# Performance work log

Measured on AMD Instinct MI355X. Metric: run time of the kernel, lower is better.

## Reference

```python
import jax, jax.numpy as jnp
import numpy as np
from jax import lax

E, H, V, S, T, B = 128, 254, 32000, 50, 50, 64


def setup_inputs() -> dict:
    key = jax.random.key(0)
    ks = jax.random.split(key, 14)
    sc = 0.05
    n = lambda k, shape: jax.random.normal(k, shape, dtype=jnp.float32) * sc
    return {
        "src": jax.random.randint(ks[0], (S, B), 0, V),
        "trg": jax.random.randint(ks[1], (T, B), 0, V),
        "emb_enc": n(ks[2], (V, E)),
        "W_ih_e": n(ks[3], (3 * H, E)),
        "W_hh_e": n(ks[4], (3 * H, H)),
        "b_ih_e": n(ks[5], (3 * H,)),
        "b_hh_e": n(ks[6], (3 * H,)),
        "emb_dec": n(ks[7], (V, E)),
        "W_ih_d": n(ks[8], (3 * H, E + H)),
        "W_hh_d": n(ks[9], (3 * H, H)),
        "b_ih_d": n(ks[10], (3 * H,)),
        "b_hh_d": n(ks[11], (3 * H,)),
        "W_out": n(ks[12], (V, E + 2 * H)),
        "b_out": n(ks[13], (V,)),
    }


def _gru_cell(x, h, W_ih, W_hh, b_ih, b_hh):
    # PyTorch GRU cell: gates ordered [r, z, n]
    gi = x @ W_ih.T + b_ih            # [B, 3H]
    gh = h @ W_hh.T + b_hh            # [B, 3H]
    i_r, i_z, i_n = jnp.split(gi, 3, axis=-1)
    h_r, h_z, h_n = jnp.split(gh, 3, axis=-1)
    r = jax.nn.sigmoid(i_r + h_r)
    z = jax.nn.sigmoid(i_z + h_z)
    n = jnp.tanh(i_n + r * h_n)
    return (1.0 - z) * n + z * h


def reference(src, trg, emb_enc, W_ih_e, W_hh_e, b_ih_e, b_hh_e,
              emb_dec, W_ih_d, W_hh_d, b_ih_d, b_hh_d, W_out, b_out):
    dt = emb_enc.dtype
    # --- Encoder: GRU over src (dropout = identity in eval) ---
    enc_emb = emb_enc[src]                       # [S, B, E]
    h0 = jnp.zeros((B, H), dtype=dt)

    def enc_step(h, x):
        h2 = _gru_cell(x, h, W_ih_e, W_hh_e, b_ih_e, b_hh_e)
        return h2, None

    context, _ = lax.scan(enc_step, h0, enc_emb)  # [B, H]

    # --- Decoder: teacher forcing (ratio=1.0) => scan over trg[:-1] ---
    dec_emb = emb_dec[trg[:-1]]                  # [T-1, B, E]

    def dec_step(h, e):
        xc = jnp.concatenate([e, context], axis=-1)          # [B, E+H]
        h2 = _gru_cell(xc, h, W_ih_d, W_hh_d, b_ih_d, b_hh_d)
        feat = jnp.concatenate([h2, context, e], axis=-1)    # [B, E+2H]
        pred = feat @ W_out.T + b_out                        # [B, V]
        return h2, pred

    _, preds = lax.scan(dec_step, context, dec_emb)  # [T-1, B, V]
    outputs = jnp.concatenate(
        [jnp.zeros((1, B, V), dtype=preds.dtype), preds], axis=0)  # [T, B, V]
    return outputs
```

## Files before the change

### kernel.cpp

```cpp
#include <hip/hip_runtime.h>
#include <cstdint>
#include <cstddef>

typedef unsigned short u16;
typedef unsigned int u32;
typedef __attribute__((ext_vector_type(8))) short bf16x8;
typedef __attribute__((ext_vector_type(4))) float f32x4;

#define AS1 __attribute__((address_space(1)))
#define AS3 __attribute__((address_space(3)))

__device__ __forceinline__ float bf2f(u16 u){ u32 x = ((u32)u)<<16; float f; __builtin_memcpy(&f,&x,4); return f; }
__device__ __forceinline__ u16 f2bf(float f){ u32 x; __builtin_memcpy(&x,&f,4); u32 r=(x+0x7FFFu+((x>>16)&1u))>>16; return (u16)r; }

__device__ __forceinline__ float fast_sig(float x){
  return __fdividef(1.f, 1.f + __expf(-x));
}
__device__ __forceinline__ float fast_tanh(float x){
  float e = __expf(2.f*x);
  return 1.f - __fdividef(2.f, e + 1.f);
}

__device__ __forceinline__ void dev_store_u16(u16* p, u16 v){
  __hip_atomic_store(p, v, __ATOMIC_RELAXED, __HIP_MEMORY_SCOPE_AGENT);
}
__device__ __forceinline__ void dev_store_u32(u32* p, u32 v){
  __hip_atomic_store(p, v, __ATOMIC_RELAXED, __HIP_MEMORY_SCOPE_AGENT);
}


__global__ void zero_bytes(uint4* p, size_t n16){
  size_t i = (size_t)blockIdx.x*blockDim.x + threadIdx.x;
  size_t st = (size_t)gridDim.x*blockDim.x;
  uint4 z; z.x=0u; z.y=0u; z.z=0u; z.w=0u;
  for (; i<n16; i+=st) p[i]=z;
}

__global__ void pad_convert_g(const float* __restrict__ src, int src_ld, int c0, int vcols,
                              u16* __restrict__ dst, int dcols){
  int i = blockIdx.x*256 + threadIdx.x;
  int tot = 768*dcols;
  if (i >= tot) return;
  int p = i/dcols, c = i - p*dcols;
  int wv = p/96, rem = p - wv*96, sec = rem>>5, u = rem&31;
  int j = wv*32 + u;
  float v = 0.f;
  if (j < 254 && c < vcols) v = src[(size_t)(sec*254 + j)*src_ld + c0 + c];
  dst[i] = f2bf(v);
}

__global__ void pad_bias_comb(const float* __restrict__ ih, const float* __restrict__ hh,
                              float* __restrict__ dst){
  int p = blockIdx.x*256 + threadIdx.x;
  if (p >= 768) return;
  int wv = p/96, rem = p - wv*96, sec = rem>>5, u = rem&31;
  int j = wv*32 + u;
  float v = 0.f;
  if (j < 254){ v = ih[sec*254 + j]; if (sec < 2) v += hh[sec*254 + j]; }
  dst[p] = v;
}

__global__ void pad_bias_g(const float* __restrict__ src, float* __restrict__ dst){
  int p = blockIdx.x*256 + threadIdx.x;
  if (p >= 768) return;
  int wv = p/96, rem = p - wv*96, sec = rem>>5, u = rem&31;
  int j = wv*32 + u;
  dst[p] = (j<254) ? src[sec*254 + j] : 0.f;
}

__global__ void gather_enc(const int* __restrict__ idx, const float* __restrict__ emb, u16* __restrict__ dst){
  int i = blockIdx.x*256 + threadIdx.x;
  int r = i>>7, k = i&127;
  dst[i] = f2bf(emb[(size_t)idx[r]*128 + k]);
}

__global__ void gather_dec(const int* __restrict__ idx, const float* __restrict__ emb,
                           u16* __restrict__ dst, u16* __restrict__ feat){
  int i = blockIdx.x*256 + threadIdx.x;
  int r = i>>7, k = i&127;
  u16 v = 0;
  if (r < 3136) v = f2bf(emb[(size_t)idx[r]*128 + k]);
  dst[i] = v;
  if (r < 3136) feat[(size_t)r*640 + 508 + k] = v;
}


__global__ __launch_bounds__(256) void gemm_bt16(
  const u16* __restrict__ A, int lda,
  const u16* __restrict__ B, int ldb,
  u16* __restrict__ C, long long ldc,
  const float* __restrict__ bias,
  int K, int Mtiles, int Mstore)
{
  __shared__ __align__(16) u16 Abuf[2][128*64];
  __shared__ __align__(16) u16 Bbuf[2][128*64];
  const int t = threadIdx.x;
  const int w = t>>6, l = t&63;
  const int wm = w>>1, wn = w&1;
  const int mt = blockIdx.x % Mtiles, nt = blockIdx.x / Mtiles;
  const int m0 = mt<<7, n0 = nt<<7;

  const int lr = l>>3, lg = l&7;

  auto stage = [&](const u16* __restrict__ G, int ld, int base0, int k0, u16* Lbuf){
    #pragma unroll
    for (int i=0;i<4;++i){
      const int rbase = i*32 + w*8;
      const int r = rbase + lr;
      const int gsw = lg ^ (r&7);
      __builtin_amdgcn_global_load_lds(
        (const AS1 void*)(G + (size_t)(base0+r)*ld + k0 + gsw*8),
        (AS3 void*)(Lbuf + rbase*64), 16, 0, 0);
    }
  };

  f32x4 acc[4][4] = {};
  const int ksteps = K>>6;

  stage(A, lda, m0, 0, Abuf[0]);
  stage(B, ldb, n0, 0, Bbuf[0]);
  asm volatile("s_waitcnt vmcnt(0)" ::: "memory");
  __syncthreads();

  for (int ks=0; ks<ksteps; ++ks){
    const int cb = ks&1;
    if (ks+1 < ksteps){
      stage(A, lda, m0, (ks+1)<<6, Abuf[cb^1]);
      stage(B, ldb, n0, (ks+1)<<6, Bbuf[cb^1]);
    }
    const u16* Al = Abuf[cb];
    const u16* Bl = Bbuf[cb];
    #pragma unroll
    for (int kk=0;kk<2;++kk){
      const int ko = kk*32 + (l>>4)*8;
      bf16x8 af[4], bfr[4];
      #pragma unroll
      for (int m=0;m<4;++m){
        const int row = wm*64+m*16+(l&15);
        af[m] = *(const bf16x8*)&Al[row*64 + (ko ^ ((row&7)<<3))];
      }
      #pragma unroll
      for (int n=0;n<4;++n){
        const int row = wn*64+n*16+(l&15);
        bfr[n] = *(const bf16x8*)&Bl[row*64 + (ko ^ ((row&7)<<3))];
      }
      #pragma unroll
      for (int m=0;m<4;++m)
        #pragma unroll
        for (int n=0;n<4;++n)
          acc[m][n] = __builtin_amdgcn_mfma_f32_16x16x32_bf16(af[m], bfr[n], acc[m][n], 0,0,0);
    }
    asm volatile("s_waitcnt vmcnt(0)" ::: "memory");
    __syncthreads();
  }

  float bv[4];
  #pragma unroll
  for (int n=0;n<4;++n) bv[n] = bias[n0 + wn*64 + n*16 + (l&15)];
  #pragma unroll
  for (int m=0;m<4;++m){
    const int rb = m0 + wm*64 + m*16 + (l>>4)*4;
    #pragma unroll
    for (int n=0;n<4;++n){
      const int col = n0 + wn*64 + n*16 + (l&15);
      #pragma unroll
      for (int r=0;r<4;++r){
        const int rr = rb + r;
        if (rr < Mstore) C[(size_t)rr*ldc + col] = f2bf(acc[m][n][r] + bv[n]);
      }
    }
  }
}


__global__ __launch_bounds__(512,1) void fused_scan_gemm(
  const u16* Whhe, const u16* Whhd, const u16* Wihdc,
  const float* bhhe, const float* bhhd,
  const u16* enc_gi, const u16* dec_gi,
  u16* feat, u16* wout_b, const float* W_out,
  float* Cg, const float* b_out, u32* ctr)
{
  __shared__ __align__(16) char smem[115200];
  const int t = threadIdx.x;
  const int w = t>>6, l = t&63;

  if (blockIdx.x < 4){
    const int g = blockIdx.x;
    const int la = l&15, q = l>>4;
    const int brow0 = g*16;

    u16* hb   = (u16*)smem;
    u16* gib  = (u16*)(smem + 16896);
    u16* ctxb = (u16*)(smem + 90624);

    bf16x8 Bf[48];

    auto loadW = [&](const u16* __restrict__ W){
      #pragma unroll
      for (int nt=0; nt<6; ++nt)
        #pragma unroll
        for (int kk=0; kk<8; ++kk)
          Bf[nt*8+kk] = *(const bf16x8*)&W[(size_t)(w*96 + nt*16 + la)*256 + kk*32 + q*8];
    };

    auto stage = [&](const u16* __restrict__ gsrc, int step, u16* dstL){
      const u16* src = gsrc + (size_t)(step*64 + brow0)*768;
      #pragma unroll
      for (int i=0;i<3;++i){
        const int off = i*4096 + w*512;
        __builtin_amdgcn_global_load_lds((const AS1 void*)(src + off + l*8),
                                         (AS3 void*)(dstL + off), 16, 0, 0);
      }
    };

    auto mm = [&](const u16* hsrc, f32x4* acc){
      #pragma unroll
      for (int kk=0; kk<8; ++kk){
        bf16x8 a = *(const bf16x8*)&hsrc[la*264 + kk*32 + q*8];
        #pragma unroll
        for (int nt=0; nt<6; ++nt)
          acc[nt] = __builtin_amdgcn_mfma_f32_16x16x32_bf16(a, Bf[nt*8+kk], acc[nt], 0,0,0);
      }
    };

    for (int i=t; i<2*16*264; i+=512) hb[i] = 0;
    loadW(Whhe);
    float bn[2];
    #pragma unroll
    for (int tl=0; tl<2; ++tl) bn[tl] = bhhe[w*96 + tl*16 + la + 64];
    stage(enc_gi, 0, gib);
    stage(enc_gi, 1, gib + 12288);
    asm volatile("s_waitcnt vmcnt(0) lgkmcnt(0)" ::: "memory");
    __builtin_amdgcn_s_barrier();

    #pragma unroll 1
    for (int s=0; s<50; ++s){
      const int hc = s&1;
      const u16* gcur = gib + (s%3)*12288;
      if (s+2 < 50) stage(enc_gi, s+2, gib + ((s+2)%3)*12288);
      f32x4 acc[6] = {};
      mm(hb + hc*4224, acc);
      #pragma unroll
      for (int tl=0; tl<2; ++tl){
        const int pb = w*96 + tl*16 + la;
        const int j  = w*32 + tl*16 + la;
        #pragma unroll
        for (int r=0;r<4;++r){
          const int b = q*4 + r;
          const float gir = bf2f(gcur[b*768 + pb]);
          const float giz = bf2f(gcur[b*768 + pb + 32]);
          const float gin = bf2f(gcur[b*768 + pb + 64]);
          const float ho = bf2f(hb[hc*4224 + b*264 + j]);
          const float rg = fast_sig(gir + acc[tl][r]);
          const float zg = fast_sig(giz + acc[2+tl][r]);
          const float ng = fast_tanh(gin + rg*(acc[4+tl][r] + bn[tl]));
          hb[(hc^1)*4224 + b*264 + j] = f2bf((1.f-zg)*ng + zg*ho);
        }
      }
      if (s+2 < 50) asm volatile("s_waitcnt vmcnt(3) lgkmcnt(0)" ::: "memory");
      else          asm volatile("s_waitcnt vmcnt(0) lgkmcnt(0)" ::: "memory");
      __builtin_amdgcn_s_barrier();
    }

    stage(dec_gi, 0, gib);
    stage(dec_gi, 1, gib + 12288);

    loadW(Wihdc);
    {
      f32x4 acc[6] = {};
      mm(hb, acc);
      #pragma unroll
      for (int nt=0; nt<6; ++nt)
        #pragma unroll
        for (int r=0;r<4;++r)
          ctxb[(q*4+r)*768 + w*96 + nt*16 + la] = f2bf(acc[nt][r]);
    }

    #pragma unroll 1
    for (int i=t; i<49*2048; i+=512){
      const int tt = i>>11, rem = i&2047, b = rem>>7, c2 = rem&127;
      if (c2 < 127){
        u32 v = *(const u32*)&hb[b*264 + c2*2];
        dev_store_u32((u32*)&feat[(size_t)(tt*64 + brow0 + b)*640 + 254 + c2*2], v);
      }
    }

    loadW(Whhd);
    #pragma unroll
    for (int tl=0; tl<2; ++tl) bn[tl] = bhhd[w*96 + tl*16 + la + 64];
    asm volatile("s_waitcnt vmcnt(0) lgkmcnt(0)" ::: "memory");
    __builtin_amdgcn_s_barrier();

    #pragma unroll 1
    for (int tt=0; tt<49; ++tt){
      const int hc = tt&1;
      const u16* gcur = gib + (tt%3)*12288;
      if (tt+2 < 49) stage(dec_gi, tt+2, gib + ((tt+2)%3)*12288);
      f32x4 acc[6] = {};
      mm(hb + hc*4224, acc);
      #pragma unroll
      for (int tl=0; tl<2; ++tl){
        const int pb = w*96 + tl*16 + la;
        const int j  = w*32 + tl*16 + la;
        #pragma unroll
        for (int r=0;r<4;++r){
          const int b = q*4 + r;
          const float gir = bf2f(gcur[b*768 + pb])      + bf2f(ctxb[b*768 + pb]);
          const float giz = bf2f(gcur[b*768 + pb + 32]) + bf2f(ctxb[b*768 + pb + 32]);
          const float gin = bf2f(gcur[b*768 + pb + 64]) + bf2f(ctxb[b*768 + pb + 64]);
          const float ho = bf2f(hb[hc*4224 + b*264 + j]);
          const float rg = fast_sig(gir + acc[tl][r]);
          const float zg = fast_sig(giz + acc[2+tl][r]);
          const float ng = fast_tanh(gin + rg*(acc[4+tl][r] + bn[tl]));
          const float h2 = (1.f-zg)*ng + zg*ho;
          const u16 hbv = f2bf(h2);
          hb[(hc^1)*4224 + b*264 + j] = hbv;
          if (j < 254) dev_store_u16(&feat[(size_t)(tt*64 + brow0 + b)*640 + j], hbv);
        }
      }
      if (tt+2 < 49) asm volatile("s_waitcnt vmcnt(11) lgkmcnt(0)" ::: "memory");
      else           asm volatile("s_waitcnt vmcnt(8) lgkmcnt(0)"  ::: "memory");
      __builtin_amdgcn_s_barrier();
      if (t==0) dev_store_u32(&ctr[g], (u32)tt);
    }
    asm volatile("s_waitcnt vmcnt(0)" ::: "memory");
    __syncthreads();
    if (t==0) dev_store_u32(&ctr[g], 49u);
    return;
  }

  const int bg = blockIdx.x - 4;
  const int wm = w>>2, wn = w&3;
  const int la = l&15, q = l>>4;
  const int lr = l>>3, lg = l&7;

  u16* AL = (u16*)smem;
  u16* BL = (u16*)(smem + 32768);

  if (bg < 125){
    const int n0c = bg<<8;
    #pragma unroll 1
    for (int i=t; i<256*80; i+=512){
      const int r = i/80, c8 = (i - r*80)<<3;
      u16 o[8];
      #pragma unroll
      for (int jj=0;jj<8;++jj){
        const int c = c8 + jj;
        o[jj] = (c < 636) ? f2bf(W_out[(size_t)(n0c+r)*636 + c]) : (u16)0;
      }
      u32* dst = (u32*)&wout_b[(size_t)(n0c+r)*640 + c8];
      const u32* sv = (const u32*)o;
      #pragma unroll
      for (int jj=0;jj<4;++jj) dev_store_u32(&dst[jj], sv[jj]);
    }
    asm volatile("s_waitcnt vmcnt(0)" ::: "memory");
    __syncthreads();
    if (t==0) dev_store_u32(&ctr[32 + bg], 1u);
  }

  const int nsleep = 1 + (bg&3);
  #pragma unroll 1
  for (int tau = bg; tau < 3125; tau += 248){
    const int mt = tau/125, nt = tau - mt*125;
    const int m0 = mt<<7, n0 = nt<<8;
    const u32 need = (u32)((2*mt+2 < 49) ? (2*mt+2) : 49);

    if (w==0){
      int cnt = 0;
      while (true){
        u32 v  = (l<4) ? __hip_atomic_load(&ctr[l], __ATOMIC_RELAXED, __HIP_MEMORY_SCOPE_AGENT) : 0xFFFFFFFFu;
        u32 wf = (l==4) ? __hip_atomic_load(&ctr[32 + nt], __ATOMIC_RELAXED, __HIP_MEMORY_SCOPE_AGENT) : 1u;
        if (__all((int)((v >= need) && (wf != 0u)))) break;
        for (int z=0; z<nsleep; ++z) __builtin_amdgcn_s_sleep(16);
        if (++cnt > (1<<22)) break;
      }
    }
    __syncthreads();

    auto stageA = [&](int k0, int buf){
      #pragma unroll
      for (int i=0;i<2;++i){
        const int rbase = i*64 + w*8;
        const int r = rbase + lr;
        __builtin_amdgcn_global_load_lds(
          (const AS1 void*)(feat + (size_t)(m0+r)*640 + k0 + ((lg^lr)<<3)),
          (AS3 void*)(AL + buf*8192 + rbase*64), 16, 0, 0);
      }
    };
    auto stageB = [&](int k0, int buf){
      #pragma unroll
      for (int i=0;i<4;++i){
        const int rbase = i*64 + w*8;
        const int r = rbase + lr;
        __builtin_amdgcn_global_load_lds(
          (const AS1 void*)(wout_b + (size_t)(n0+r)*640 + k0 + ((lg^lr)<<3)),
          (AS3 void*)(BL + buf*16384 + rbase*64), 16, 0, 0);
      }
    };

    f32x4 acc[4][4] = {};
    stageA(0,0); stageB(0,0);
    asm volatile("s_waitcnt vmcnt(0)" ::: "memory");
    __syncthreads();

    #pragma unroll 1
    for (int ks=0; ks<10; ++ks){
      const int cb = ks&1;
      if (ks < 9){ stageA((ks+1)<<6, cb^1); stageB((ks+1)<<6, cb^1); }
      const u16* Alp = AL + cb*8192;
      const u16* Blp = BL + cb*16384;
      #pragma unroll
      for (int kk=0;kk<2;++kk){
        const int ko = kk*32 + q*8;
        bf16x8 af[4], bfr[4];
        #pragma unroll
        for (int m=0;m<4;++m){
          const int row = wm*64 + m*16 + la;
          af[m] = *(const bf16x8*)&Alp[row*64 + (ko ^ ((row&7)<<3))];
        }
        #pragma unroll
        for (int n=0;n<4;++n){
          const int row = wn*64 + n*16 + la;
          bfr[n] = *(const bf16x8*)&Blp[row*64 + (ko ^ ((row&7)<<3))];
        }
        #pragma unroll
        for (int m=0;m<4;++m)
          #pragma unroll
          for (int n=0;n<4;++n)
            acc[m][n] = __builtin_amdgcn_mfma_f32_16x16x32_bf16(af[m], bfr[n], acc[m][n], 0,0,0);
      }
      asm volatile("s_waitcnt vmcnt(0)" ::: "memory");
      __syncthreads();
    }

    float bv[4];
    #pragma unroll
    for (int n=0;n<4;++n) bv[n] = b_out[n0 + wn*64 + n*16 + la];
    #pragma unroll
    for (int m=0;m<4;++m){
      const int rb = m0 + wm*64 + m*16 + q*4;
      #pragma unroll
      for (int n=0;n<4;++n){
        const int col = n0 + wn*64 + n*16 + la;
        #pragma unroll
        for (int r=0;r<4;++r){
          const int rr = rb + r;
          if (rr < 3136)
            __builtin_nontemporal_store(acc[m][n][r] + bv[n], &Cg[(size_t)rr*32000 + col]);
        }
      }
    }
  }
}


extern "C" void kernel_launch(void* const* d_in, const int* in_sizes, int n_in,
                              void* d_out, int out_size, void* d_ws, size_t ws_size,
                              hipStream_t stream) {
  const int*   src     = (const int*)d_in[0];
  const int*   trg     = (const int*)d_in[1];
  const float* emb_enc = (const float*)d_in[2];
  const float* W_ih_e  = (const float*)d_in[3];
  const float* W_hh_e  = (const float*)d_in[4];
  const float* b_ih_e  = (const float*)d_in[5];
  const float* b_hh_e  = (const float*)d_in[6];
  const float* emb_dec = (const float*)d_in[7];
  const float* W_ih_d  = (const float*)d_in[8];
  const float* W_hh_d  = (const float*)d_in[9];
  const float* b_ih_d  = (const float*)d_in[10];
  const float* b_hh_d  = (const float*)d_in[11];
  const float* W_out   = (const float*)d_in[12];
  const float* b_out   = (const float*)d_in[13];
  float* out = (float*)d_out;

  char* basep = (char*)d_ws;
  size_t off = 0;
  auto take = [&](size_t b)->char*{ char* p = basep + off; off = (off + b + 255) & ~(size_t)255; return p; };
  u16* feat    = (u16*)take(4096000);
  u32* ctr     = (u32*)take(4096);
  u16* wout_b  = (u16*)take(40960000);
  u16* wihe_b  = (u16*)take(196608);
  u16* wihde_b = (u16*)take(196608);
  u16* wihdc_b = (u16*)take(393216);
  u16* whhe_b  = (u16*)take(393216);
  u16* whhd_b  = (u16*)take(393216);
  u16* encx_b  = (u16*)take(819200);
  u16* dece_b  = (u16*)take(819200);
  u16* enc_gi  = (u16*)take(4915200);
  u16* dec_gi  = (u16*)take(4915200);
  float* bihe_p = (float*)take(3072);
  float* bihd_p = (float*)take(3072);
  float* bhhe_p = (float*)take(3072);
  float* bhhd_p = (float*)take(3072);
  (void)in_sizes; (void)n_in; (void)out_size; (void)ws_size;

  zero_bytes<<<1, 256, 0, stream>>>((uint4*)ctr, (size_t)(4096/16));
  zero_bytes<<<2000, 256, 0, stream>>>((uint4*)out, (size_t)(8192000/16));

  pad_convert_g<<<384, 256, 0, stream>>>(W_ih_e, 128,   0, 128, wihe_b, 128);
  pad_convert_g<<<384, 256, 0, stream>>>(W_ih_d, 382,   0, 128, wihde_b, 128);
  pad_convert_g<<<768, 256, 0, stream>>>(W_ih_d, 382, 128, 254, wihdc_b, 256);
  pad_convert_g<<<768, 256, 0, stream>>>(W_hh_e, 254,   0, 254, whhe_b, 256);
  pad_convert_g<<<768, 256, 0, stream>>>(W_hh_d, 254,   0, 254, whhd_b, 256);

  pad_bias_comb<<<3, 256, 0, stream>>>(b_ih_e, b_hh_e, bihe_p);
  pad_bias_comb<<<3, 256, 0, stream>>>(b_ih_d, b_hh_d, bihd_p);
  pad_bias_g<<<3, 256, 0, stream>>>(b_hh_e, bhhe_p);
  pad_bias_g<<<3, 256, 0, stream>>>(b_hh_d, bhhd_p);

  gather_enc<<<1600, 256, 0, stream>>>(src, emb_enc, encx_b);
  gather_dec<<<1600, 256, 0, stream>>>(trg, emb_dec, dece_b, feat);

  gemm_bt16<<<25*6, 256, 0, stream>>>(encx_b, 128, wihe_b, 128, enc_gi, (long long)768, bihe_p, 128, 25, 3200);
  gemm_bt16<<<25*6, 256, 0, stream>>>(dece_b, 128, wihde_b, 128, dec_gi, (long long)768, bihd_p, 128, 25, 3200);

  fused_scan_gemm<<<252, 512, 0, stream>>>(whhe_b, whhd_b, wihdc_b, bhhe_p, bhhd_p,
                                           enc_gi, dec_gi, feat, wout_b, W_out,
                                           out + (size_t)64*32000, b_out, ctr);
}
```

Measured before the change: 518.3 us.

## Transpose input-gate precompute layout and batch feature stores out of GRU recurrence

The input-projection GEMMs now produce gate pre-activations transposed (gate-major, [768 x 3200]) with bias applied per row, so the recurrent blocks can stage them and read four batch values per lane as one vector load. The decoder context projection is folded into dec_gi once before the recurrence, which removes the per-step context reads and frees LDS. The hidden state is carried in registers instead of being re-read from LDS. Per-element feature stores are replaced by one wide 64-bit copy of the previous step's hidden row, issued early in the next step. The cost is an extra pass over dec_gi in global memory before the decoder loop, and the waitcnt bookkeeping becomes tighter.

```diff
diff --git a/kernel.cpp b/kernel.cpp
--- a/kernel.cpp
+++ b/kernel.cpp
@@ -4,8 +4,10 @@
 
 typedef unsigned short u16;
 typedef unsigned int u32;
+typedef unsigned long long u64;
 typedef __attribute__((ext_vector_type(8))) short bf16x8;
 typedef __attribute__((ext_vector_type(4))) float f32x4;
+typedef __attribute__((ext_vector_type(4))) unsigned short u16x4;
 
 #define AS1 __attribute__((address_space(1)))
 #define AS3 __attribute__((address_space(3)))
@@ -25,6 +27,9 @@
   __hip_atomic_store(p, v, __ATOMIC_RELAXED, __HIP_MEMORY_SCOPE_AGENT);
 }
 __device__ __forceinline__ void dev_store_u32(u32* p, u32 v){
+  __hip_atomic_store(p, v, __ATOMIC_RELAXED, __HIP_MEMORY_SCOPE_AGENT);
+}
+__device__ __forceinline__ void dev_store_u64(u64* p, u64 v){
   __hip_atomic_store(p, v, __ATOMIC_RELAXED, __HIP_MEMORY_SCOPE_AGENT);
 }
 
@@ -154,19 +159,19 @@
     __syncthreads();
   }
 
-  float bv[4];
-  #pragma unroll
-  for (int n=0;n<4;++n) bv[n] = bias[n0 + wn*64 + n*16 + (l&15)];
   #pragma unroll
   for (int m=0;m<4;++m){
     const int rb = m0 + wm*64 + m*16 + (l>>4)*4;
     #pragma unroll
-    for (int n=0;n<4;++n){
-      const int col = n0 + wn*64 + n*16 + (l&15);
-      #pragma unroll
-      for (int r=0;r<4;++r){
-        const int rr = rb + r;
-        if (rr < Mstore) C[(size_t)rr*ldc + col] = f2bf(acc[m][n][r] + bv[n]);
+    for (int r=0;r<4;++r){
+      const int rr = rb + r;
+      if (rr < Mstore){
+        const float bvr = bias[rr];
+        #pragma unroll
+        for (int n=0;n<4;++n){
+          const int col = n0 + wn*64 + n*16 + (l&15);
+          C[(size_t)rr*ldc + col] = f2bf(acc[m][n][r] + bvr);
+        }
       }
     }
   }
@@ -176,11 +181,11 @@
 __global__ __launch_bounds__(512,1) void fused_scan_gemm(
   const u16* Whhe, const u16* Whhd, const u16* Wihdc,
   const float* bhhe, const float* bhhd,
-  const u16* enc_gi, const u16* dec_gi,
+  const u16* enc_gi, u16* dec_gi,
   u16* feat, u16* wout_b, const float* W_out,
   float* Cg, const float* b_out, u32* ctr)
 {
-  __shared__ __align__(16) char smem[115200];
+  __shared__ __align__(16) char smem[98304];
   const int t = threadIdx.x;
   const int w = t>>6, l = t&63;
 
@@ -189,9 +194,8 @@
     const int la = l&15, q = l>>4;
     const int brow0 = g*16;
 
-    u16* hb   = (u16*)smem;
-    u16* gib  = (u16*)(smem + 16896);
-    u16* ctxb = (u16*)(smem + 90624);
+    u16* hb  = (u16*)smem;
+    u16* gib = (u16*)(smem + 16896);
 
     bf16x8 Bf[48];
 
@@ -204,12 +208,14 @@
     };
 
     auto stage = [&](const u16* __restrict__ gsrc, int step, u16* dstL){
-      const u16* src = gsrc + (size_t)(step*64 + brow0)*768;
+      const int colbase = step*64 + brow0 + ((l&1)<<3);
       #pragma unroll
       for (int i=0;i<3;++i){
-        const int off = i*4096 + w*512;
-        __builtin_amdgcn_global_load_lds((const AS1 void*)(src + off + l*8),
-                                         (AS3 void*)(dstL + off), 16, 0, 0);
+        const int rbase = (w*3 + i)*32;
+        const int row = rbase + (l>>1);
+        __builtin_amdgcn_global_load_lds(
+          (const AS1 void*)(gsrc + (size_t)row*3200 + colbase),
+          (AS3 void*)(dstL + rbase*16), 16, 0, 0);
       }
     };
 
@@ -228,6 +234,7 @@
     float bn[2];
     #pragma unroll
     for (int tl=0; tl<2; ++tl) bn[tl] = bhhe[w*96 + tl*16 + la + 64];
+    float hreg[8] = {};
     stage(enc_gi, 0, gib);
     stage(enc_gi, 1, gib + 12288);
     asm volatile("s_waitcnt vmcnt(0) lgkmcnt(0)" ::: "memory");
@@ -236,25 +243,26 @@
     #pragma unroll 1
     for (int s=0; s<50; ++s){
       const int hc = s&1;
-      const u16* gcur = gib + (s%3)*12288;
+      const u16* gT = gib + (s%3)*12288;
       if (s+2 < 50) stage(enc_gi, s+2, gib + ((s+2)%3)*12288);
       f32x4 acc[6] = {};
       mm(hb + hc*4224, acc);
       #pragma unroll
       for (int tl=0; tl<2; ++tl){
-        const int pb = w*96 + tl*16 + la;
+        const int pr = w*96 + tl*16 + la;
         const int j  = w*32 + tl*16 + la;
+        u16x4 g_r = *(const u16x4*)&gT[pr*16 + q*4];
+        u16x4 g_z = *(const u16x4*)&gT[(pr+32)*16 + q*4];
+        u16x4 g_n = *(const u16x4*)&gT[(pr+64)*16 + q*4];
         #pragma unroll
         for (int r=0;r<4;++r){
           const int b = q*4 + r;
-          const float gir = bf2f(gcur[b*768 + pb]);
-          const float giz = bf2f(gcur[b*768 + pb + 32]);
-          const float gin = bf2f(gcur[b*768 + pb + 64]);
-          const float ho = bf2f(hb[hc*4224 + b*264 + j]);
-          const float rg = fast_sig(gir + acc[tl][r]);
-          const float zg = fast_sig(giz + acc[2+tl][r]);
-          const float ng = fast_tanh(gin + rg*(acc[4+tl][r] + bn[tl]));
-          hb[(hc^1)*4224 + b*264 + j] = f2bf((1.f-zg)*ng + zg*ho);
+          const float rg = fast_sig(bf2f(g_r[r]) + acc[tl][r]);
+          const float zg = fast_sig(bf2f(g_z[r]) + acc[2+tl][r]);
+          const float ng = fast_tanh(bf2f(g_n[r]) + rg*(acc[4+tl][r] + bn[tl]));
+          const float h2 = (1.f-zg)*ng + zg*hreg[tl*4+r];
+          hreg[tl*4+r] = h2;
+          hb[(hc^1)*4224 + b*264 + j] = f2bf(h2);
         }
       }
       if (s+2 < 50) asm volatile("s_waitcnt vmcnt(3) lgkmcnt(0)" ::: "memory");
@@ -262,10 +270,8 @@
       __builtin_amdgcn_s_barrier();
     }
 
-    stage(dec_gi, 0, gib);
-    stage(dec_gi, 1, gib + 12288);
-
     loadW(Wihdc);
+    u16* ctxT = gib + 2*12288;
     {
       f32x4 acc[6] = {};
       mm(hb, acc);
@@ -273,8 +279,31 @@
       for (int nt=0; nt<6; ++nt)
         #pragma unroll
         for (int r=0;r<4;++r)
-          ctxb[(q*4+r)*768 + w*96 + nt*16 + la] = f2bf(acc[nt][r]);
-    }
+          ctxT[(w*96 + nt*16 + la)*16 + q*4 + r] = f2bf(acc[nt][r]);
+    }
+    asm volatile("s_waitcnt lgkmcnt(0)" ::: "memory");
+    __builtin_amdgcn_s_barrier();
+
+    #pragma unroll 1
+    for (int idx=t; idx<768*49; idx+=512){
+      const int p = idx/49, tt2 = idx - p*49;
+      u16* gp = dec_gi + (size_t)p*3200 + tt2*64 + brow0;
+      uint4 a0 = *(uint4*)gp, a1 = *((uint4*)gp + 1);
+      uint4 c0 = *(uint4*)&ctxT[p*16], c1 = *((uint4*)&ctxT[p*16] + 1);
+      auto addbf = [](u32 x, u32 y)->u32{
+        u32 lo = (u32)f2bf(bf2f((u16)(x&0xffff)) + bf2f((u16)(y&0xffff)));
+        u32 hi = (u32)f2bf(bf2f((u16)(x>>16))    + bf2f((u16)(y>>16)));
+        return lo | (hi<<16);
+      };
+      a0.x=addbf(a0.x,c0.x); a0.y=addbf(a0.y,c0.y); a0.z=addbf(a0.z,c0.z); a0.w=addbf(a0.w,c0.w);
+      a1.x=addbf(a1.x,c1.x); a1.y=addbf(a1.y,c1.y); a1.z=addbf(a1.z,c1.z); a1.w=addbf(a1.w,c1.w);
+      *(uint4*)gp = a0; *((uint4*)gp + 1) = a1;
+    }
+    asm volatile("s_waitcnt vmcnt(0)" ::: "memory");
+    __builtin_amdgcn_s_barrier();
+
+    stage(dec_gi, 0, gib);
+    stage(dec_gi, 1, gib + 12288);
 
     #pragma unroll 1
     for (int i=t; i<49*2048; i+=512){
@@ -294,34 +323,50 @@
     #pragma unroll 1
     for (int tt=0; tt<49; ++tt){
       const int hc = tt&1;
-      const u16* gcur = gib + (tt%3)*12288;
+      const u16* gT = gib + (tt%3)*12288;
+      if (tt >= 1){
+        #pragma unroll
+        for (int i0=t; i0<1024; i0+=512){
+          const int b = i0>>6, c = i0&63;
+          const u16* hrow = hb + hc*4224 + b*264;
+          u16* frow = feat + (size_t)((tt-1)*64 + brow0 + b)*640;
+          if (c < 63) dev_store_u64((u64*)(frow + c*4), *(const u64*)(hrow + c*4));
+          else        dev_store_u32((u32*)(frow + 252), *(const u32*)(hrow + 252));
+        }
+      }
       if (tt+2 < 49) stage(dec_gi, tt+2, gib + ((tt+2)%3)*12288);
       f32x4 acc[6] = {};
       mm(hb + hc*4224, acc);
       #pragma unroll
       for (int tl=0; tl<2; ++tl){
-        const int pb = w*96 + tl*16 + la;
+        const int pr = w*96 + tl*16 + la;
         const int j  = w*32 + tl*16 + la;
+        u16x4 g_r = *(const u16x4*)&gT[pr*16 + q*4];
+        u16x4 g_z = *(const u16x4*)&gT[(pr+32)*16 + q*4];
+        u16x4 g_n = *(const u16x4*)&gT[(pr+64)*16 + q*4];
         #pragma unroll
         for (int r=0;r<4;++r){
           const int b = q*4 + r;
-          const float gir = bf2f(gcur[b*768 + pb])      + bf2f(ctxb[b*768 + pb]);
-          const float giz = bf2f(gcur[b*768 + pb + 32]) + bf2f(ctxb[b*768 + pb + 32]);
-          const float gin = bf2f(gcur[b*768 + pb + 64]) + bf2f(ctxb[b*768 + pb + 64]);
-          const float ho = bf2f(hb[hc*4224 + b*264 + j]);
-          const float rg = fast_sig(gir + acc[tl][r]);
-          const float zg = fast_sig(giz + acc[2+tl][r]);
-          const float ng = fast_tanh(gin + rg*(acc[4+tl][r] + bn[tl]));
-          const float h2 = (1.f-zg)*ng + zg*ho;
-          const u16 hbv = f2bf(h2);
-          hb[(hc^1)*4224 + b*264 + j] = hbv;
-          if (j < 254) dev_store_u16(&feat[(size_t)(tt*64 + brow0 + b)*640 + j], hbv);
-        }
-      }
-      if (tt+2 < 49) asm volatile("s_waitcnt vmcnt(11) lgkmcnt(0)" ::: "memory");
-      else           asm volatile("s_waitcnt vmcnt(8) lgkmcnt(0)"  ::: "memory");
+          const float rg = fast_sig(bf2f(g_r[r]) + acc[tl][r]);
+          const float zg = fast_sig(bf2f(g_z[r]) + acc[2+tl][r]);
+          const float ng = fast_tanh(bf2f(g_n[r]) + rg*(acc[4+tl][r] + bn[tl]));
+          const float h2 = (1.f-zg)*ng + zg*hreg[tl*4+r];
+          hreg[tl*4+r] = h2;
+          hb[(hc^1)*4224 + b*264 + j] = f2bf(h2);
+        }
+      }
+      if (tt+2 < 49) asm volatile("s_waitcnt vmcnt(3) lgkmcnt(0)" ::: "memory");
+      else           asm volatile("s_waitcnt vmcnt(0) lgkmcnt(0)" ::: "memory");
       __builtin_amdgcn_s_barrier();
       if (t==0) dev_store_u32(&ctr[g], (u32)tt);
+    }
+    #pragma unroll
+    for (int i0=t; i0<1024; i0+=512){
+      const int b = i0>>6, c = i0&63;
+      const u16* hrow = hb + 4224 + b*264;
+      u16* frow = feat + (size_t)(48*64 + brow0 + b)*640;
+      if (c < 63) dev_store_u64((u64*)(frow + c*4), *(const u64*)(hrow + c*4));
+      else        dev_store_u32((u32*)(frow + 252), *(const u32*)(hrow + 252));
     }
     asm volatile("s_waitcnt vmcnt(0)" ::: "memory");
     __syncthreads();
@@ -511,8 +556,8 @@
   gather_enc<<<1600, 256, 0, stream>>>(src, emb_enc, encx_b);
   gather_dec<<<1600, 256, 0, stream>>>(trg, emb_dec, dece_b, feat);
 
-  gemm_bt16<<<25*6, 256, 0, stream>>>(encx_b, 128, wihe_b, 128, enc_gi, (long long)768, bihe_p, 128, 25, 3200);
-  gemm_bt16<<<25*6, 256, 0, stream>>>(dece_b, 128, wihde_b, 128, dec_gi, (long long)768, bihd_p, 128, 25, 3200);
+  gemm_bt16<<<6*25, 256, 0, stream>>>(wihe_b, 128, encx_b, 128, enc_gi, (long long)3200, bihe_p, 128, 6, 768);
+  gemm_bt16<<<6*25, 256, 0, stream>>>(wihde_b, 128, dece_b, 128, dec_gi, (long long)3200, bihd_p, 128, 6, 768);
 
   fused_scan_gemm<<<252, 512, 0, stream>>>(whhe_b, whhd_b, wihdc_b, bhhe_p, bhhd_p,
                                            enc_gi, dec_gi, feat, wout_b, W_out,
```

New measurement: 721.1 us. 1.39x slower.
